# Optimization experiments

Measured on AMD Instinct MI355X. Metric: run time of the kernel, lower is better.

## Reference

```python
import jax, jax.numpy as jnp
import numpy as np
from jax import lax


def _lstm_dir(x_gates, Whh, bhh, reverse):
    # x_gates: (B,T,4H) = x @ Wih.T + bih, precomputed for all timesteps
    B, T, G = x_gates.shape
    H = G // 4

    def step(carry, xg):
        h, c = carry
        g = xg + h @ Whh.T + bhh
        i, f, gg, o = jnp.split(g, 4, axis=-1)  # PyTorch gate order i,f,g,o
        c = jax.nn.sigmoid(f) * c + jax.nn.sigmoid(i) * jnp.tanh(gg)
        h = jax.nn.sigmoid(o) * jnp.tanh(c)
        return (h, c), h

    xs = jnp.swapaxes(x_gates, 0, 1)  # (T,B,4H)
    if reverse:
        xs = xs[::-1]
    init = (jnp.zeros((B, H), x_gates.dtype), jnp.zeros((B, H), x_gates.dtype))
    _, hs = lax.scan(step, init, xs)
    if reverse:
        hs = hs[::-1]
    return jnp.swapaxes(hs, 0, 1)  # (B,T,H)


def _forward(embeddings, mask,
             enc_Wih_f, enc_Whh_f, enc_bih_f, enc_bhh_f,
             enc_Wih_b, enc_Whh_b, enc_bih_b, enc_bhh_b,
             attn_W, attn_b, tag_embed,
             dec_Wih, dec_Whh, dec_bih, dec_bhh,
             Wout, bout):
    B, T, D = embeddings.shape
    maskf = mask.astype(embeddings.dtype)

    # --- bidirectional encoder ---
    xg_f = jnp.einsum('btd,gd->btg', embeddings, enc_Wih_f) + enc_bih_f
    xg_b = jnp.einsum('btd,gd->btg', embeddings, enc_Wih_b) + enc_bih_b
    out_f = _lstm_dir(xg_f, enc_Whh_f, enc_bhh_f, False)
    out_b = _lstm_dir(xg_b, enc_Whh_b, enc_bhh_b, True)
    output = jnp.concatenate([out_f, out_b], axis=-1) * maskf[:, :, None]  # (B,T,2H)

    lengths = mask.sum(axis=1) - 1
    last_output = output[jnp.arange(B), lengths]  # (B,2H)

    def attend(v):
        # AllenNLP BilinearAttention: softmax(v @ W @ M^T + b), then * mask
        sc = jnp.einsum('bd,de,bte->bt', v, attn_W, output) + attn_b
        return jax.nn.softmax(sc, axis=-1) * maskf

    context0 = jnp.einsum('bt,btd->bd', attend(last_output), output)  # (B,2H)

    Hd = output.shape[-1]          # decoder hidden = 2H
    E = tag_embed.shape[1]         # tag embedding dim (== hidden_size)
    h0 = jnp.zeros((B, Hd), embeddings.dtype)
    c0 = jnp.zeros((B, Hd), embeddings.dtype)

    def step(carry, xt):
        h, c, context, last_tag = carry
        aligned, i = xt
        emb = jnp.where(i == 0,
                        jnp.zeros((B, E), embeddings.dtype),
                        tag_embed[last_tag])
        dec_input = jnp.concatenate([emb, context, aligned], axis=-1)  # (B, E+4H)
        g = dec_input @ dec_Wih.T + dec_bih + h @ dec_Whh.T + dec_bhh
        ii, f, gg, o = jnp.split(g, 4, axis=-1)
        c = jax.nn.sigmoid(f) * c + jax.nn.sigmoid(ii) * jnp.tanh(gg)
        h = jax.nn.sigmoid(o) * jnp.tanh(c)
        concated = jnp.concatenate([h, context], axis=-1)  # (B,4H)
        score = concated @ Wout.T + bout                   # (B,V)
        new_context = jnp.einsum('bt,btd->bd', attend(h), output)
        last_tag = jnp.argmax(score, axis=-1).astype(jnp.int32)
        return (h, c, new_context, last_tag), score

    xs = (jnp.swapaxes(output, 0, 1), jnp.arange(T))
    init = (h0, c0, context0, jnp.zeros((B,), jnp.int32))
    _, scores = lax.scan(step, init, xs)  # (T,B,V)
    return jnp.swapaxes(scores, 0, 1)     # (B,T,V) slot logits


def setup_inputs() -> dict:
    key = jax.random.key(0)
    B, T, D, H, E, V = 32, 64, 512, 512, 512, 2048
    H2 = 2 * H
    dec_in = E + 2 * H2  # tag_emb + context(2H) + aligned(2H)
    ks = jax.random.split(key, 20)
    s = 0.02
    f32 = jnp.float32
    return {
        'embeddings': jax.random.normal(ks[0], (B, T, D), f32),
        'mask': jnp.ones((B, T), jnp.int32),
        'enc_Wih_f': jax.random.normal(ks[1], (4 * H, D), f32) * s,
        'enc_Whh_f': jax.random.normal(ks[2], (4 * H, H), f32) * s,
        'enc_bih_f': jax.random.normal(ks[3], (4 * H,), f32) * s,
        'enc_bhh_f': jax.random.normal(ks[4], (4 * H,), f32) * s,
        'enc_Wih_b': jax.random.normal(ks[5], (4 * H, D), f32) * s,
        'enc_Whh_b': jax.random.normal(ks[6], (4 * H, H), f32) * s,
        'enc_bih_b': jax.random.normal(ks[7], (4 * H,), f32) * s,
        'enc_bhh_b': jax.random.normal(ks[8], (4 * H,), f32) * s,
        'attn_W': jax.random.normal(ks[9], (H2, H2), f32) * s,
        'attn_b': jax.random.normal(ks[10], (), f32) * s,
        'tag_embed': jax.random.normal(ks[11], (V, E), f32) * s,
        'dec_Wih': jax.random.normal(ks[12], (4 * H2, dec_in), f32) * s,
        'dec_Whh': jax.random.normal(ks[13], (4 * H2, H2), f32) * s,
        'dec_bih': jax.random.normal(ks[14], (4 * H2,), f32) * s,
        'dec_bhh': jax.random.normal(ks[15], (4 * H2,), f32) * s,
        'Wout': jax.random.normal(ks[16], (V, 2 * H2), f32) * s,
        'bout': jax.random.normal(ks[17], (V,), f32) * s,
    }


def reference(embeddings, mask,
              enc_Wih_f, enc_Whh_f, enc_bih_f, enc_bhh_f,
              enc_Wih_b, enc_Whh_b, enc_bih_b, enc_bhh_b,
              attn_W, attn_b, tag_embed,
              dec_Wih, dec_Whh, dec_bih, dec_bhh,
              Wout, bout):
    return _forward(embeddings, mask,
                    enc_Wih_f, enc_Whh_f, enc_bih_f, enc_bhh_f,
                    enc_Wih_b, enc_Whh_b, enc_bih_b, enc_bhh_b,
                    attn_W, attn_b, tag_embed,
                    dec_Wih, dec_Whh, dec_bih, dec_bhh,
                    Wout, bout)
```

## Files before the change

### kernel.cpp

```cpp
#include <hip/hip_runtime.h>

#define B   32
#define T   64
#define D   512
#define H   512
#define H2  1024
#define G4  4096
#define V   2048
#define DEC_IN 2560

__device__ __forceinline__ float sigm(float x) { return 1.f / (1.f + expf(-x)); }

__device__ __forceinline__ unsigned fenc(float f) {
  unsigned u = __float_as_uint(f);
  return (u & 0x80000000u) ? ~u : (u | 0x80000000u);
}

__device__ __forceinline__ void st_wt(float* p, float v) {
  __hip_atomic_store(p, v, __ATOMIC_RELAXED, __HIP_MEMORY_SCOPE_AGENT);
}

__device__ __forceinline__ void pbar(unsigned* slots, unsigned* flags, int myid, int nblk) {
  __syncthreads();
  if (threadIdx.x == 0)
    __hip_atomic_store(slots + myid, 1u, __ATOMIC_RELAXED, __HIP_MEMORY_SCOPE_AGENT);
  if (myid == 0) {
    for (int s = threadIdx.x; s < nblk; s += 256) {
      while (!__hip_atomic_load(slots + s, __ATOMIC_RELAXED, __HIP_MEMORY_SCOPE_AGENT))
        __builtin_amdgcn_s_sleep(1);
    }
    __syncthreads();
    if (threadIdx.x < 16)
      __hip_atomic_store(flags + threadIdx.x*16, 1u, __ATOMIC_RELAXED, __HIP_MEMORY_SCOPE_AGENT);
  }
  if (threadIdx.x == 0) {
    unsigned* f = flags + (myid & 15)*16;
    while (!__hip_atomic_load(f, __ATOMIC_RELAXED, __HIP_MEMORY_SCOPE_AGENT))
      __builtin_amdgcn_s_sleep(1);
    (void)__hip_atomic_load(f, __ATOMIC_ACQUIRE, __HIP_MEMORY_SCOPE_AGENT);
  }
  __syncthreads();
}

__global__ __launch_bounds__(256) void gemm_nt(
    const float* __restrict__ A, int lda,
    const float* __restrict__ W, int ldw,
    float* __restrict__ C, int ldc,
    const float* __restrict__ bias0, const float* __restrict__ bias1,
    int K)
{
  __shared__ float As[16][132];
  __shared__ float Ws[16][68];
  const int tid = threadIdx.x;
  const int nb = blockIdx.x * 64;
  const int mb = blockIdx.y * 128;
  const int tx = tid & 15;
  const int ty = tid >> 4;
  float acc[8][4] = {};

  const int am = tid >> 1, ak = (tid & 1) * 8;
  const int wn = tid >> 2, wk = (tid & 3) * 4;
  const float* aptr = A + (size_t)(mb + am) * lda + ak;
  const float* wptr = W + (size_t)(nb + wn) * ldw + wk;

  for (int k0 = 0; k0 < K; k0 += 16) {
    float4 u = *(const float4*)(aptr + k0);
    float4 v = *(const float4*)(aptr + k0 + 4);
    float4 w = *(const float4*)(wptr + k0);
    As[ak+0][am] = u.x; As[ak+1][am] = u.y; As[ak+2][am] = u.z; As[ak+3][am] = u.w;
    As[ak+4][am] = v.x; As[ak+5][am] = v.y; As[ak+6][am] = v.z; As[ak+7][am] = v.w;
    Ws[wk+0][wn] = w.x; Ws[wk+1][wn] = w.y; Ws[wk+2][wn] = w.z; Ws[wk+3][wn] = w.w;
    __syncthreads();
    #pragma unroll
    for (int k = 0; k < 16; ++k) {
      float4 a0 = *(const float4*)&As[k][ty*8];
      float4 a1 = *(const float4*)&As[k][ty*8+4];
      float4 wv = *(const float4*)&Ws[k][tx*4];
      float av[8] = {a0.x,a0.y,a0.z,a0.w,a1.x,a1.y,a1.z,a1.w};
      #pragma unroll
      for (int i = 0; i < 8; ++i) {
        acc[i][0] += av[i]*wv.x; acc[i][1] += av[i]*wv.y;
        acc[i][2] += av[i]*wv.z; acc[i][3] += av[i]*wv.w;
      }
    }
    __syncthreads();
  }
  float b4[4];
  #pragma unroll
  for (int j = 0; j < 4; ++j) {
    float bv = 0.f;
    if (bias0) bv += bias0[nb + tx*4 + j];
    if (bias1) bv += bias1[nb + tx*4 + j];
    b4[j] = bv;
  }
  #pragma unroll
  for (int i = 0; i < 8; ++i) {
    float4 o;
    o.x = acc[i][0] + b4[0]; o.y = acc[i][1] + b4[1];
    o.z = acc[i][2] + b4[2]; o.w = acc[i][3] + b4[3];
    *(float4*)&C[(size_t)(mb + ty*8 + i) * ldc + nb + tx*4] = o;
  }
}

__device__ void attend_slice(int ab, int aslice, const float* __restrict__ hvec,
                             float* __restrict__ ctxdst,
                             const float* __restrict__ outbuf, const float* __restrict__ projo,
                             const int* __restrict__ mask, float* scratch, int tid)
{
  float* scp = scratch;
  float* scv = scratch + 256;
  float* p2  = scratch + 320;
  const int tq = tid >> 2, dq = tid & 3;
  const float4* hv = (const float4*)(hvec + dq*256);
  const float4* pv = (const float4*)(projo + (size_t)(ab*T + tq)*H2 + dq*256);
  float p = 0.f;
  #pragma unroll 8
  for (int k4 = 0; k4 < 64; ++k4) {
    float4 a = hv[k4], q = pv[k4];
    p += a.x*q.x + a.y*q.y + a.z*q.z + a.w*q.w;
  }
  scp[tid] = p;
  __syncthreads();
  if (tid < 64) {
    float v = scp[tid*4] + scp[tid*4+1] + scp[tid*4+2] + scp[tid*4+3];
    float mx = v;
    #pragma unroll
    for (int d = 32; d; d >>= 1) mx = fmaxf(mx, __shfl_xor(mx, d, 64));
    float e = expf(v - mx);
    float sm = e;
    #pragma unroll
    for (int d = 32; d; d >>= 1) sm += __shfl_xor(sm, d, 64);
    scv[tid] = e * (1.f / sm) * (float)mask[ab*T + tid];
  }
  __syncthreads();
  {
    const int dl = tid & 127, th = tid >> 7;
    const int dg = aslice*128 + dl;
    float acc = 0.f;
    #pragma unroll 8
    for (int q = 0; q < 32; ++q) {
      int tt = th*32 + q;
      acc += scv[tt] * outbuf[(size_t)(ab*T + tt)*H2 + dg];
    }
    if (th == 1) p2[dl] = acc;
    __syncthreads();
    if (th == 0) st_wt(&ctxdst[dg*32 + ab], acc + p2[dl]);
  }
}

__global__ __launch_bounds__(256, 1) void encoder_persistent(
    const float* __restrict__ xg_f, const float* __restrict__ xg_b,
    const float* __restrict__ Whh_f, const float* __restrict__ Whh_b,
    const int* __restrict__ mask,
    float* __restrict__ hencT,
    float* __restrict__ outbuf,
    unsigned* __restrict__ eslots, unsigned* __restrict__ eflags)
{
  __shared__ float S_lds[2][128*36];
  __shared__ float pacc[2048];
  __shared__ float g_lds[512];
  const int blk = blockIdx.x, tid = threadIdx.x;
  const int lane = tid & 63, wv = tid >> 6;
  const int dir = blk >> 7, nd = blk & 127;
  const int hibase = nd * 4;
  const int jj = tid & 7, kk = tid >> 3;
  const float* xg  = dir ? xg_b : xg_f;
  const float* Whh = dir ? Whh_b : Whh_f;
  float* hbase = hencT + dir * 32768;

  float wge[2][16];
  #pragma unroll
  for (int p = 0; p < 2; ++p) {
    int jl = jj*2 + p;
    int j = (jl>>2)*512 + hibase + (jl&3);
    #pragma unroll
    for (int sc = 0; sc < 4; ++sc)
      #pragma unroll
      for (int i = 0; i < 4; ++i)
        wge[p][sc*4+i] = Whh[(size_t)j*512 + sc*128 + i*32 + kk];
  }
  float c_reg = 0.f;
  const int kr = tid >> 1, bh = (tid & 1) * 16;

  for (int tt = 0; tt < 64; ++tt) {
    const int t = dir ? (63 - tt) : tt;
    const float* hc = hbase + (tt & 1) * 16384;
    float* hn = hbase + ((tt + 1) & 1) * 16384;

    float a0[32], a1[32];
    #pragma unroll
    for (int q = 0; q < 32; ++q) { a0[q] = 0.f; a1[q] = 0.f; }

    float4 rr0, rr1, rr2, rr3;
    {
      const float4* p = (const float4*)(hc + kr*32 + bh);
      rr0 = p[0]; rr1 = p[1]; rr2 = p[2]; rr3 = p[3];
      float* d = &S_lds[0][kr*36 + bh];
      *(float4*)d = rr0; *(float4*)(d+4) = rr1; *(float4*)(d+8) = rr2; *(float4*)(d+12) = rr3;
    }
    __syncthreads();
    #pragma unroll
    for (int sc = 0; sc < 4; ++sc) {
      if (sc < 3) {
        const float4* p = (const float4*)(hc + (sc+1)*4096 + kr*32 + bh);
        rr0 = p[0]; rr1 = p[1]; rr2 = p[2]; rr3 = p[3];
      }
      const float* Sb = &S_lds[sc & 1][0];
      #pragma unroll
      for (int i = 0; i < 4; ++i) {
        const float* sp = Sb + (i*32 + kk)*36;
        float w0 = wge[0][sc*4+i], w1 = wge[1][sc*4+i];
        #pragma unroll
        for (int q = 0; q < 8; ++q) {
          float4 s4 = *(const float4*)(sp + q*4);
          a0[q*4+0] += w0*s4.x; a0[q*4+1] += w0*s4.y; a0[q*4+2] += w0*s4.z; a0[q*4+3] += w0*s4.w;
          a1[q*4+0] += w1*s4.x; a1[q*4+1] += w1*s4.y; a1[q*4+2] += w1*s4.z; a1[q*4+3] += w1*s4.w;
        }
      }
      if (sc < 3) {
        float* d = &S_lds[(sc+1) & 1][kr*36 + bh];
        *(float4*)d = rr0; *(float4*)(d+4) = rr1; *(float4*)(d+8) = rr2; *(float4*)(d+12) = rr3;
      }
      __syncthreads();
    }
    #pragma unroll
    for (int dd = 8; dd <= 32; dd <<= 1) {
      #pragma unroll
      for (int q = 0; q < 32; ++q) {
        a0[q] += __shfl_down(a0[q], dd, 64);
        a1[q] += __shfl_down(a1[q], dd, 64);
      }
    }
    if (lane < 8) {
      float* pw = &pacc[wv*512 + lane*64];
      #pragma unroll
      for (int q = 0; q < 32; ++q) { pw[q] = a0[q]; pw[32+q] = a1[q]; }
    }
    __syncthreads();
    #pragma unroll
    for (int r = 0; r < 2; ++r) {
      int o = tid + r*256;
      int jl = o >> 5, b = o & 31;
      int off = (jl>>1)*64 + (jl&1)*32 + b;
      float v = pacc[off] + pacc[512+off] + pacc[1024+off] + pacc[1536+off];
      v += xg[(size_t)(b*T + t)*2048 + (jl>>2)*512 + hibase + (jl&3)];
      g_lds[jl*32 + b] = v;
    }
    __syncthreads();
    if (tid < 128) {
      int hil = tid >> 5, b = tid & 31;
      float gi = g_lds[(0*4+hil)*32 + b];
      float gf = g_lds[(1*4+hil)*32 + b];
      float gg = g_lds[(2*4+hil)*32 + b];
      float go = g_lds[(3*4+hil)*32 + b];
      c_reg = sigm(gf)*c_reg + sigm(gi)*tanhf(gg);
      float h = sigm(go)*tanhf(c_reg);
      int hi = hibase + hil;
      st_wt(&hn[hi*32 + b], h);
      st_wt(&outbuf[(size_t)(b*T + t)*H2 + dir*512 + hi], h * (float)mask[b*T + t]);
    }
    pbar(eslots + (dir*64 + tt)*128, eflags + (dir*64 + tt)*256, nd, 128);
  }
}

#define GROW1(lr) (8*wv + ((lr) < 8 ? (lr) : 24 + (lr)))
#define GROW2(lr) (16*wv + (lr))
#define SLDG(qq, s) { int krr = (s)*64 + GROW1(lrow); \
  const float* bs = (krr < 1024) ? (hTc + krr*32) : (ctxc + (krr-1024)*32); \
  qq##a = *(const float4*)(bs + scol2); qq##b = *(const float4*)(bs + scol2 + 4); }
#define SLDS(qq, s) { int krr = (s)*64 + GROW2(lrow); \
  const float* bs = (krr < 1024) ? (hTn + krr*32) : (ctxc + (krr-1024)*32); \
  qq##a = *(const float4*)(bs + scol2); qq##b = *(const float4*)(bs + scol2 + 4); }
#define STW(qq, BUF) { float* d = Sw + (BUF)*576 + lrow*36 + scol2; \
  *(float4*)d = qq##a; *(float4*)(d+4) = qq##b; }
#define COMPG(sl, BUF) { const float* Sb = Sw + (BUF)*576; \
  _Pragma("unroll") for (int i = 0; i < 2; ++i) { \
    float w0 = Wg[jl0*2052 + (sl)*64 + i*32 + kkg]; \
    float w1 = Wg[jl1*2052 + (sl)*64 + i*32 + kkg]; \
    const float* sp = Sb + (i*8 + kkl)*36; \
    _Pragma("unroll") for (int q = 0; q < 8; ++q) { \
      float4 s4 = *(const float4*)(sp + q*4); \
      a0[q*4+0] += w0*s4.x; a0[q*4+1] += w0*s4.y; a0[q*4+2] += w0*s4.z; a0[q*4+3] += w0*s4.w; \
      a1[q*4+0] += w1*s4.x; a1[q*4+1] += w1*s4.y; a1[q*4+2] += w1*s4.z; a1[q*4+3] += w1*s4.w; } } }
#define COMPS(sl, BUF) { const float* sp = Sw + (BUF)*576 + lrow*36; \
  float w0 = ws0[sl], w1 = ws1[sl]; \
  _Pragma("unroll") for (int q = 0; q < 8; ++q) { \
    float4 s4 = *(const float4*)(sp + q*4); \
    a0[q*4+0] += w0*s4.x; a0[q*4+1] += w0*s4.y; a0[q*4+2] += w0*s4.z; a0[q*4+3] += w0*s4.w; \
    a1[q*4+0] += w1*s4.x; a1[q*4+1] += w1*s4.y; a1[q*4+2] += w1*s4.z; a1[q*4+3] += w1*s4.w; } }

__global__ __launch_bounds__(256, 1) void decoder_persistent(
    const float* __restrict__ basep, const float* __restrict__ tagp,
    const float* __restrict__ dWhh,  const float* __restrict__ dWih,
    const float* __restrict__ Wout,  const float* __restrict__ bout,
    const float* __restrict__ projo, const float* __restrict__ outbuf,
    const int* __restrict__ mask,
    float* __restrict__ hT,
    float* __restrict__ ctxT,
    float* __restrict__ hrow,
    unsigned long long* __restrict__ argslot,
    unsigned* __restrict__ dslots, unsigned* __restrict__ dflags,
    float* __restrict__ out)
{
  extern __shared__ float dyn[];
  float* Wg    = dyn;
  float* S2    = dyn + 32832;
  float* pacc  = dyn + 37440;
  float* g_lds = dyn + 39488;

  const int blk = blockIdx.x, tid = threadIdx.x;
  const int lane = tid & 63, wv = tid >> 6;
  const int hibase = blk * 4;
  const int jj = lane & 7, kkl = lane >> 3;
  const int kkg = 8*wv + kkl;
  const int jl0 = jj*2, jl1 = jj*2 + 1;
  const int vv = tid & 3, kq = tid >> 2;
  const int vbase = blk * 8;
  const int lrow = lane >> 2, scol2 = (lane & 3) * 8;
  const int ab = blk & 31, aslice = blk >> 5;
  float* Sw = S2 + wv*1152;

  for (int jl = 0; jl < 16; ++jl) {
    int j = (jl>>2)*1024 + hibase + (jl&3);
    #pragma unroll
    for (int r = 0; r < 2; ++r) {
      int c = tid*4 + r*1024;
      float4 w;
      if (c < 1024) w = *(const float4*)(dWhh + (size_t)j*1024 + c);
      else          w = *(const float4*)(dWih + (size_t)j*2560 + 512 + (c - 1024));
      *(float4*)&Wg[jl*2052 + c] = w;
    }
  }
  float ws0[32], ws1[32];
  {
    int v0 = vbase + vv*2;
    #pragma unroll
    for (int s2 = 0; s2 < 32; ++s2) {
      ws0[s2] = Wout[(size_t)(v0+0)*2048 + s2*64 + kq];
      ws1[s2] = Wout[(size_t)(v0+1)*2048 + s2*64 + kq];
    }
  }

  float c_reg = 0.f;
  int bslot = 0;

  {
    int len = -1;
    for (int i = 0; i < T; ++i) len += mask[ab*T + i];
    attend_slice(ab, aslice, outbuf + (size_t)(ab*T + len)*H2, ctxT,
                 outbuf, projo, mask, pacc, tid);
  }
  pbar(dslots + (bslot)*256, dflags + (bslot)*256, blk, 256); bslot++;

  for (int t = 0; t < T; ++t) {
    const int cur = t & 1, nxt = cur ^ 1;
    const float* hTc  = hT + cur*32768;
    float*       hTn  = hT + nxt*32768;
    const float* ctxc = ctxT + cur*32768;
    float*       ctxn = ctxT + nxt*32768;

    const int b_own = tid & 31;
    const int jlA = tid >> 5, jlB = jlA + 8;
    const int jA = (jlA>>2)*1024 + hibase + (jlA&3);
    const int jB = (jlB>>2)*1024 + hibase + (jlB&3);
    float extA = basep[(size_t)(b_own*T + t)*G4 + jA];
    float extB = basep[(size_t)(b_own*T + t)*G4 + jB];
    if (t > 0) {
      unsigned long long sl64 = __hip_atomic_load(&argslot[((t+2)%3)*32 + b_own],
                                                  __ATOMIC_RELAXED, __HIP_MEMORY_SCOPE_AGENT);
      unsigned tg = ~(unsigned)sl64;
      extA += tagp[(size_t)tg*G4 + jA];
      extB += tagp[(size_t)tg*G4 + jB];
    }

    float a0[32], a1[32];
    #pragma unroll
    for (int q = 0; q < 32; ++q) { a0[q] = 0.f; a1[q] = 0.f; }
    {
      float4 q0a,q0b,q1a,q1b,q2a,q2b,q3a,q3b;
      SLDG(q0, 0) SLDG(q1, 1) SLDG(q2, 2) SLDG(q3, 3)
      STW(q0, 0)
      for (int g = 0; g < 8; ++g) {
        const int sl = g*4;
        if (sl+4 < 32) SLDG(q0, sl+4)
        COMPG(sl, 0)
        STW(q1, 1)
        if (sl+5 < 32) SLDG(q1, sl+5)
        COMPG(sl+1, 1)
        STW(q2, 0)
        if (sl+6 < 32) SLDG(q2, sl+6)
        COMPG(sl+2, 0)
        STW(q3, 1)
        if (sl+7 < 32) SLDG(q3, sl+7)
        COMPG(sl+3, 1)
        if (sl+4 < 32) STW(q0, 0)
      }
    }
    #pragma unroll
    for (int dd = 8; dd <= 32; dd <<= 1) {
      #pragma unroll
      for (int q = 0; q < 32; ++q) {
        a0[q] += __shfl_down(a0[q], dd, 64);
        a1[q] += __shfl_down(a1[q], dd, 64);
      }
    }
    if (lane < 8) {
      float* pw = &pacc[wv*512 + lane*64];
      #pragma unroll
      for (int q = 0; q < 32; ++q) { pw[q] = a0[q]; pw[32+q] = a1[q]; }
    }
    __syncthreads();
    #pragma unroll
    for (int r = 0; r < 2; ++r) {
      int o = tid + r*256;
      int jl = o >> 5, b = o & 31;
      int off = (jl>>1)*64 + (jl&1)*32 + b;
      float vsum = pacc[off] + pacc[512+off] + pacc[1024+off] + pacc[1536+off];
      vsum += (r == 0) ? extA : extB;
      g_lds[jl*32 + b] = vsum;
    }
    __syncthreads();
    if (tid < 128) {
      int hil = tid >> 5, b = tid & 31;
      float gi = g_lds[(0*4+hil)*32 + b];
      float gf = g_lds[(1*4+hil)*32 + b];
      float gg = g_lds[(2*4+hil)*32 + b];
      float go = g_lds[(3*4+hil)*32 + b];
      c_reg = sigm(gf)*c_reg + sigm(gi)*tanhf(gg);
      float h = sigm(go)*tanhf(c_reg);
      int hi = hibase + hil;
      st_wt(&hTn[hi*32 + b], h);
      st_wt(&hrow[b*1024 + hi], h);
    }
    pbar(dslots + (bslot)*256, dflags + (bslot)*256, blk, 256); bslot++;

    #pragma unroll
    for (int q = 0; q < 32; ++q) { a0[q] = 0.f; a1[q] = 0.f; }
    {
      float4 q0a,q0b,q1a,q1b,q2a,q2b,q3a,q3b;
      SLDS(q0, 0) SLDS(q1, 1) SLDS(q2, 2) SLDS(q3, 3)
      STW(q0, 0)
      #pragma unroll
      for (int g = 0; g < 8; ++g) {
        const int sl = g*4;
        if (sl+4 < 32) SLDS(q0, sl+4)
        COMPS(sl, 0)
        STW(q1, 1)
        if (sl+5 < 32) SLDS(q1, sl+5)
        COMPS(sl+1, 1)
        STW(q2, 0)
        if (sl+6 < 32) SLDS(q2, sl+6)
        COMPS(sl+2, 0)
        STW(q3, 1)
        if (sl+7 < 32) SLDS(q3, sl+7)
        COMPS(sl+3, 1)
        if (sl+4 < 32) STW(q0, 0)
      }
    }
    #pragma unroll
    for (int dd = 4; dd <= 32; dd <<= 1) {
      #pragma unroll
      for (int q = 0; q < 32; ++q) {
        a0[q] += __shfl_down(a0[q], dd, 64);
        a1[q] += __shfl_down(a1[q], dd, 64);
      }
    }
    if (lane < 4) {
      float* pw = &pacc[wv*256 + lane*64];
      #pragma unroll
      for (int q = 0; q < 32; ++q) { pw[q] = a0[q]; pw[32+q] = a1[q]; }
    }
    __syncthreads();
    {
      int vl = tid & 7, b = tid >> 3;
      int off = (vl>>1)*64 + (vl&1)*32 + b;
      float s = pacc[off] + pacc[256+off] + pacc[512+off] + pacc[768+off];
      s += bout[vbase + vl];
      st_wt(&out[(size_t)(b*T + t)*V + vbase + vl], s);
      g_lds[vl*32 + b] = s;
    }
    __syncthreads();
    if (tid < 32) {
      int b = tid;
      float best = g_lds[b]; int bi = 0;
      #pragma unroll
      for (int vl = 1; vl < 8; ++vl) {
        float s = g_lds[vl*32 + b];
        if (s > best) { best = s; bi = vl; }
      }
      unsigned long long e = ((unsigned long long)fenc(best) << 32)
                           | (unsigned long long)(unsigned)(~(unsigned)(vbase + bi));
      atomicMax(&argslot[(t%3)*32 + b], e);
    } else if (blk == 0 && tid >= 32 && tid < 64) {
      __hip_atomic_store(&argslot[((t+1)%3)*32 + (tid - 32)], 0ull,
                         __ATOMIC_RELAXED, __HIP_MEMORY_SCOPE_AGENT);
    }
    if (t < 63) {
      __syncthreads();
      attend_slice(ab, aslice, hrow + ab*1024, ctxn, outbuf, projo, mask, pacc, tid);
    }
    pbar(dslots + (bslot)*256, dflags + (bslot)*256, blk, 256); bslot++;
  }
}

extern "C" void kernel_launch(void* const* d_in, const int* in_sizes, int n_in,
                              void* d_out, int out_size, void* d_ws, size_t ws_size,
                              hipStream_t stream)
{
  (void)in_sizes; (void)n_in; (void)out_size; (void)ws_size;
  const float* emb    = (const float*)d_in[0];
  const int*   mask   = (const int*)d_in[1];
  const float* Wih_f  = (const float*)d_in[2];
  const float* Whh_f  = (const float*)d_in[3];
  const float* bih_f  = (const float*)d_in[4];
  const float* bhh_f  = (const float*)d_in[5];
  const float* Wih_b  = (const float*)d_in[6];
  const float* Whh_b  = (const float*)d_in[7];
  const float* bih_b  = (const float*)d_in[8];
  const float* bhh_b  = (const float*)d_in[9];
  const float* attnW  = (const float*)d_in[10];
  const float* tagemb = (const float*)d_in[12];
  const float* dWih   = (const float*)d_in[13];
  const float* dWhh   = (const float*)d_in[14];
  const float* dbih   = (const float*)d_in[15];
  const float* dbhh   = (const float*)d_in[16];
  const float* Wout   = (const float*)d_in[17];
  const float* bout   = (const float*)d_in[18];
  float* out = (float*)d_out;

  float* ws = (float*)d_ws;
  float* xg_f   = ws + 0;
  float* xg_b   = ws + 4194304;
  float* outbuf = ws + 8388608;
  float* projo  = ws + 10485760;
  float* basep  = ws + 12582912;
  float* tagp   = ws + 20971520;
  float* hT     = ws + 29360128;
  float* ctxT   = ws + 29425664;
  float* hrow   = ws + 29491200;
  float* hencT  = ws + 29523968;
  unsigned long long* argslot = (unsigned long long*)(ws + 29589504);
  unsigned* dslots = (unsigned*)(ws + 29589696);
  unsigned* dflags = (unsigned*)(ws + 29622720);
  unsigned* eslots = (unsigned*)(ws + 29655744);
  unsigned* eflags = (unsigned*)(ws + 29672128);

  (void)hipFuncSetAttribute((const void*)decoder_persistent,
                            hipFuncAttributeMaxDynamicSharedMemorySize, 160000);

  hipMemsetAsync((void*)(ws + 29360128), 0, (size_t)(29704896 - 29360128) * sizeof(float), stream);

  gemm_nt<<<dim3(32, 16), 256, 0, stream>>>(emb, 512, Wih_f, 512, xg_f, 2048, bih_f, bhh_f, 512);
  gemm_nt<<<dim3(32, 16), 256, 0, stream>>>(emb, 512, Wih_b, 512, xg_b, 2048, bih_b, bhh_b, 512);
  gemm_nt<<<dim3(64, 16), 256, 0, stream>>>(tagemb, 512, dWih, DEC_IN, tagp, G4, nullptr, nullptr, 512);
  encoder_persistent<<<256, 256, 0, stream>>>(xg_f, xg_b, Whh_f, Whh_b, mask, hencT, outbuf, eslots, eflags);
  gemm_nt<<<dim3(16, 16), 256, 0, stream>>>(outbuf, H2, attnW, H2, projo, H2, nullptr, nullptr, H2);
  gemm_nt<<<dim3(64, 16), 256, 0, stream>>>(outbuf, H2, dWih + 1536, DEC_IN, basep, G4, dbih, dbhh, H2);
  decoder_persistent<<<256, 256, 160000, stream>>>(basep, tagp, dWhh, dWih, Wout, bout,
                                                   projo, outbuf, mask, hT, ctxT, hrow,
                                                   argslot, dslots, dflags, out);
}
```

Before: 4.757 ms.

## Use per-wavefront LDS staging in encoder and widen GEMM tiles to 128x128

```diff
diff --git a/kernel.cpp b/kernel.cpp
--- a/kernel.cpp
+++ b/kernel.cpp
@@ -49,56 +49,57 @@
     const float* __restrict__ bias0, const float* __restrict__ bias1,
     int K)
 {
-  __shared__ float As[16][132];
-  __shared__ float Ws[16][68];
+  __shared__ float As[8][132];
+  __shared__ float Bs[8][132];
   const int tid = threadIdx.x;
-  const int nb = blockIdx.x * 64;
+  const int nb = blockIdx.x * 128;
   const int mb = blockIdx.y * 128;
   const int tx = tid & 15;
   const int ty = tid >> 4;
-  float acc[8][4] = {};
-
-  const int am = tid >> 1, ak = (tid & 1) * 8;
-  const int wn = tid >> 2, wk = (tid & 3) * 4;
+  float acc[8][8] = {};
+
+  const int am = tid >> 1, ak = (tid & 1) * 4;
   const float* aptr = A + (size_t)(mb + am) * lda + ak;
-  const float* wptr = W + (size_t)(nb + wn) * ldw + wk;
-
-  for (int k0 = 0; k0 < K; k0 += 16) {
-    float4 u = *(const float4*)(aptr + k0);
-    float4 v = *(const float4*)(aptr + k0 + 4);
-    float4 w = *(const float4*)(wptr + k0);
-    As[ak+0][am] = u.x; As[ak+1][am] = u.y; As[ak+2][am] = u.z; As[ak+3][am] = u.w;
-    As[ak+4][am] = v.x; As[ak+5][am] = v.y; As[ak+6][am] = v.z; As[ak+7][am] = v.w;
-    Ws[wk+0][wn] = w.x; Ws[wk+1][wn] = w.y; Ws[wk+2][wn] = w.z; Ws[wk+3][wn] = w.w;
-    __syncthreads();
-    #pragma unroll
-    for (int k = 0; k < 16; ++k) {
+  const float* bptr = W + (size_t)(nb + am) * ldw + ak;
+
+  for (int k0 = 0; k0 < K; k0 += 8) {
+    float4 av = *(const float4*)(aptr + k0);
+    float4 bv = *(const float4*)(bptr + k0);
+    As[ak+0][am] = av.x; As[ak+1][am] = av.y; As[ak+2][am] = av.z; As[ak+3][am] = av.w;
+    Bs[ak+0][am] = bv.x; Bs[ak+1][am] = bv.y; Bs[ak+2][am] = bv.z; Bs[ak+3][am] = bv.w;
+    __syncthreads();
+    #pragma unroll
+    for (int k = 0; k < 8; ++k) {
       float4 a0 = *(const float4*)&As[k][ty*8];
       float4 a1 = *(const float4*)&As[k][ty*8+4];
-      float4 wv = *(const float4*)&Ws[k][tx*4];
-      float av[8] = {a0.x,a0.y,a0.z,a0.w,a1.x,a1.y,a1.z,a1.w};
-      #pragma unroll
-      for (int i = 0; i < 8; ++i) {
-        acc[i][0] += av[i]*wv.x; acc[i][1] += av[i]*wv.y;
-        acc[i][2] += av[i]*wv.z; acc[i][3] += av[i]*wv.w;
-      }
-    }
-    __syncthreads();
-  }
-  float b4[4];
+      float4 b0 = *(const float4*)&Bs[k][tx*8];
+      float4 b1 = *(const float4*)&Bs[k][tx*8+4];
+      float avv[8] = {a0.x,a0.y,a0.z,a0.w,a1.x,a1.y,a1.z,a1.w};
+      float bvv[8] = {b0.x,b0.y,b0.z,b0.w,b1.x,b1.y,b1.z,b1.w};
+      #pragma unroll
+      for (int i = 0; i < 8; ++i)
+        #pragma unroll
+        for (int j = 0; j < 8; ++j)
+          acc[i][j] += avv[i]*bvv[j];
+    }
+    __syncthreads();
+  }
+  float b8[8];
   #pragma unroll
-  for (int j = 0; j < 4; ++j) {
-    float bv = 0.f;
-    if (bias0) bv += bias0[nb + tx*4 + j];
-    if (bias1) bv += bias1[nb + tx*4 + j];
-    b4[j] = bv;
+  for (int j = 0; j < 8; ++j) {
+    float bvv = 0.f;
+    if (bias0) bvv += bias0[nb + tx*8 + j];
+    if (bias1) bvv += bias1[nb + tx*8 + j];
+    b8[j] = bvv;
   }
   #pragma unroll
   for (int i = 0; i < 8; ++i) {
-    float4 o;
-    o.x = acc[i][0] + b4[0]; o.y = acc[i][1] + b4[1];
-    o.z = acc[i][2] + b4[2]; o.w = acc[i][3] + b4[3];
-    *(float4*)&C[(size_t)(mb + ty*8 + i) * ldc + nb + tx*4] = o;
+    float4 o0, o1;
+    o0.x = acc[i][0]+b8[0]; o0.y = acc[i][1]+b8[1]; o0.z = acc[i][2]+b8[2]; o0.w = acc[i][3]+b8[3];
+    o1.x = acc[i][4]+b8[4]; o1.y = acc[i][5]+b8[5]; o1.z = acc[i][6]+b8[6]; o1.w = acc[i][7]+b8[7];
+    size_t idx = (size_t)(mb + ty*8 + i) * ldc + nb + tx*8;
+    *(float4*)&C[idx]     = o0;
+    *(float4*)&C[idx + 4] = o1;
   }
 }
 
@@ -156,7 +157,7 @@
     float* __restrict__ outbuf,
     unsigned* __restrict__ eslots, unsigned* __restrict__ eflags)
 {
-  __shared__ float S_lds[2][128*36];
+  __shared__ float S_lds[9216];
   __shared__ float pacc[2048];
   __shared__ float g_lds[512];
   const int blk = blockIdx.x, tid = threadIdx.x;
@@ -164,9 +165,11 @@
   const int dir = blk >> 7, nd = blk & 127;
   const int hibase = nd * 4;
   const int jj = tid & 7, kk = tid >> 3;
+  const int kkl = lane >> 3;
   const float* xg  = dir ? xg_b : xg_f;
   const float* Whh = dir ? Whh_b : Whh_f;
   float* hbase = hencT + dir * 32768;
+  float* Sw = S_lds + wv*2304;
 
   float wge[2][16];
   #pragma unroll
@@ -180,7 +183,8 @@
         wge[p][sc*4+i] = Whh[(size_t)j*512 + sc*128 + i*32 + kk];
   }
   float c_reg = 0.f;
-  const int kr = tid >> 1, bh = (tid & 1) * 16;
+  const int lr = lane >> 1, halfc = (lane & 1) * 16;
+  const int grow = (lr >> 3)*32 + 8*wv + (lr & 7);
 
   for (int tt = 0; tt < 64; ++tt) {
     const int t = dir ? (63 - tt) : tt;
@@ -191,24 +195,23 @@
     #pragma unroll
     for (int q = 0; q < 32; ++q) { a0[q] = 0.f; a1[q] = 0.f; }
 
-    float4 rr0, rr1, rr2, rr3;
+    float4 r0, r1, r2, r3;
     {
-      const float4* p = (const float4*)(hc + kr*32 + bh);
-      rr0 = p[0]; rr1 = p[1]; rr2 = p[2]; rr3 = p[3];
-      float* d = &S_lds[0][kr*36 + bh];
-      *(float4*)d = rr0; *(float4*)(d+4) = rr1; *(float4*)(d+8) = rr2; *(float4*)(d+12) = rr3;
-    }
-    __syncthreads();
+      const float4* p = (const float4*)(hc + grow*32 + halfc);
+      r0 = p[0]; r1 = p[1]; r2 = p[2]; r3 = p[3];
+      float* d = Sw + lr*36 + halfc;
+      *(float4*)d = r0; *(float4*)(d+4) = r1; *(float4*)(d+8) = r2; *(float4*)(d+12) = r3;
+    }
     #pragma unroll
     for (int sc = 0; sc < 4; ++sc) {
       if (sc < 3) {
-        const float4* p = (const float4*)(hc + (sc+1)*4096 + kr*32 + bh);
-        rr0 = p[0]; rr1 = p[1]; rr2 = p[2]; rr3 = p[3];
-      }
-      const float* Sb = &S_lds[sc & 1][0];
+        const float4* p = (const float4*)(hc + ((sc+1)*128 + grow)*32 + halfc);
+        r0 = p[0]; r1 = p[1]; r2 = p[2]; r3 = p[3];
+      }
+      const float* Sb = Sw + (sc & 1)*1152;
       #pragma unroll
       for (int i = 0; i < 4; ++i) {
-        const float* sp = Sb + (i*32 + kk)*36;
+        const float* sp = Sb + (i*8 + kkl)*36;
         float w0 = wge[0][sc*4+i], w1 = wge[1][sc*4+i];
         #pragma unroll
         for (int q = 0; q < 8; ++q) {
@@ -218,10 +221,9 @@
         }
       }
       if (sc < 3) {
-        float* d = &S_lds[(sc+1) & 1][kr*36 + bh];
-        *(float4*)d = rr0; *(float4*)(d+4) = rr1; *(float4*)(d+8) = rr2; *(float4*)(d+12) = rr3;
-      }
-      __syncthreads();
+        float* d = Sw + ((sc+1) & 1)*1152 + lr*36 + halfc;
+        *(float4*)d = r0; *(float4*)(d+4) = r1; *(float4*)(d+8) = r2; *(float4*)(d+12) = r3;
+      }
     }
     #pragma unroll
     for (int dd = 8; dd <= 32; dd <<= 1) {
@@ -550,12 +552,12 @@
 
   hipMemsetAsync((void*)(ws + 29360128), 0, (size_t)(29704896 - 29360128) * sizeof(float), stream);
 
-  gemm_nt<<<dim3(32, 16), 256, 0, stream>>>(emb, 512, Wih_f, 512, xg_f, 2048, bih_f, bhh_f, 512);
-  gemm_nt<<<dim3(32, 16), 256, 0, stream>>>(emb, 512, Wih_b, 512, xg_b, 2048, bih_b, bhh_b, 512);
-  gemm_nt<<<dim3(64, 16), 256, 0, stream>>>(tagemb, 512, dWih, DEC_IN, tagp, G4, nullptr, nullptr, 512);
+  gemm_nt<<<dim3(16, 16), 256, 0, stream>>>(emb, 512, Wih_f, 512, xg_f, 2048, bih_f, bhh_f, 512);
+  gemm_nt<<<dim3(16, 16), 256, 0, stream>>>(emb, 512, Wih_b, 512, xg_b, 2048, bih_b, bhh_b, 512);
+  gemm_nt<<<dim3(32, 16), 256, 0, stream>>>(tagemb, 512, dWih, DEC_IN, tagp, G4, nullptr, nullptr, 512);
   encoder_persistent<<<256, 256, 0, stream>>>(xg_f, xg_b, Whh_f, Whh_b, mask, hencT, outbuf, eslots, eflags);
-  gemm_nt<<<dim3(16, 16), 256, 0, stream>>>(outbuf, H2, attnW, H2, projo, H2, nullptr, nullptr, H2);
-  gemm_nt<<<dim3(64, 16), 256, 0, stream>>>(outbuf, H2, dWih + 1536, DEC_IN, basep, G4, dbih, dbhh, H2);
+  gemm_nt<<<dim3(8, 16), 256, 0, stream>>>(outbuf, H2, attnW, H2, projo, H2, nullptr, nullptr, H2);
+  gemm_nt<<<dim3(32, 16), 256, 0, stream>>>(outbuf, H2, dWih + 1536, DEC_IN, basep, G4, dbih, dbhh, H2);
   decoder_persistent<<<256, 256, 160000, stream>>>(basep, tagp, dWhh, dWih, Wout, bout,
                                                    projo, outbuf, mask, hT, ctxT, hrow,
                                                    argslot, dslots, dflags, out);
```

Result: no change. 4.729 ms (-0.6%).
